# Kernel tuning notes

Measured on AMD Instinct MI355X. Metric: run time of the kernel, lower is better.

The kernel has to match this reference:

```python
import jax, jax.numpy as jnp
import numpy as np

N_NODES = 50000
N_EDGES = 500000
H = 128
C = 2


def setup_inputs() -> dict:
    key = jax.random.key(0)
    ks = jax.random.split(key, 8)
    node_repr = jax.random.normal(ks[0], (N_NODES, H), dtype=jnp.float32)
    src = jax.random.randint(ks[1], (N_EDGES,), 0, N_NODES, dtype=jnp.int32)
    dst = jax.random.randint(ks[2], (N_EDGES,), 0, N_NODES, dtype=jnp.int32)
    # Linear weights stored as (in, out); scaled like torch default init
    W1 = jax.random.normal(ks[3], (4 * H, 2 * H), dtype=jnp.float32) / np.sqrt(4 * H)
    b1 = jnp.zeros((2 * H,), dtype=jnp.float32)
    W2 = jax.random.normal(ks[4], (2 * H, H), dtype=jnp.float32) / np.sqrt(2 * H)
    b2 = jnp.zeros((H,), dtype=jnp.float32)
    W3 = jax.random.normal(ks[5], (H, C), dtype=jnp.float32) / np.sqrt(H)
    b3 = jnp.zeros((C,), dtype=jnp.float32)
    return {"node_repr": node_repr, "src": src, "dst": dst,
            "W1": W1, "b1": b1, "W2": W2, "b2": b2, "W3": W3, "b3": b3}


def reference(node_repr, src, dst, W1, b1, W2, b2, W3, b3):
    h_i = node_repr[src]                      # [E, H] gather
    h_j = node_repr[dst]                      # [E, H] gather
    diff = jnp.abs(h_i - h_j)
    product = h_i * h_j
    edge_input = jnp.concatenate([h_i, h_j, diff, product], axis=1)  # [E, 4H]
    x = jax.nn.relu(edge_input @ W1 + b1)     # [E, 2H]; dropout = identity (eval)
    x = jax.nn.relu(x @ W2 + b2)              # [E, H]
    return x @ W3 + b3                        # [E, C]
```

## Files before the change

### kernel.cpp

```cpp
#include <hip/hip_runtime.h>


#define H 128

typedef __bf16 bf16x8 __attribute__((ext_vector_type(8)));
typedef float f32x4 __attribute__((ext_vector_type(4)));

__device__ __forceinline__ unsigned short f2bf(float f) {
    unsigned u = __builtin_bit_cast(unsigned, f);
    u += 0x7FFFu + ((u >> 16) & 1u);
    return (unsigned short)(u >> 16);
}
__device__ __forceinline__ float bfhi(unsigned u) {
    return __builtin_bit_cast(float, u & 0xffff0000u);
}
__device__ __forceinline__ float bflo(unsigned u) {
    return __builtin_bit_cast(float, u << 16);
}
__device__ __forceinline__ unsigned pk2(float r0, float r1) {
    unsigned u0 = __builtin_bit_cast(unsigned, r0) + 0x8000u;
    unsigned u1 = __builtin_bit_cast(unsigned, r1) + 0x8000u;
    return __builtin_amdgcn_perm(u1, u0, 0x07060302u);
}
__device__ __forceinline__ unsigned comb(unsigned ua, unsigned ub, bool isdiff) {
    float a0 = bflo(ua), a1 = bfhi(ua);
    float b0 = bflo(ub), b1 = bfhi(ub);
    float r0 = isdiff ? fabsf(a0 - b0) : a0 * b0;
    float r1 = isdiff ? fabsf(a1 - b1) : a1 * b1;
    return pk2(r0, r1);
}
__device__ __forceinline__ unsigned short cvt1(float v) {
    unsigned u = __builtin_bit_cast(unsigned, v) + 0x8000u;
    return (unsigned short)(u >> 16);
}

__global__ void prep_node(const float* __restrict__ node, unsigned short* __restrict__ nbf) {
    int idx = blockIdx.x * 256 + threadIdx.x;
    const f32x4* p = (const f32x4*)(node) + idx;
    f32x4 v = *p;
    ushort4 w;
    w.x = f2bf(v.x); w.y = f2bf(v.y); w.z = f2bf(v.z); w.w = f2bf(v.w);
    *(ushort4*)(nbf + idx * 4) = w;
}

__global__ void prep_w1(const float* __restrict__ W1, unsigned short* __restrict__ W1P) {
    int o = blockIdx.x * 256 + threadIdx.x;
    int chunk = o >> 9;
    int g_nt = chunk >> 4;
    int ks = chunk & 15;
    int r = o & 511;
    int lane = r >> 3;
    int j = r & 7;
    int row = g_nt * 16 + (lane & 15);
    int k = ks * 32 + (lane >> 4) * 8 + j;
    W1P[o] = f2bf(W1[k * 256 + row]);
}

__global__ void prep_w2(const float* __restrict__ W2, unsigned short* __restrict__ W2P) {
    int o = blockIdx.x * 256 + threadIdx.x;
    int chunk = o >> 9;
    int g_nt = chunk >> 3;
    int ks = chunk & 7;
    int r = o & 511;
    int lane = r >> 3;
    int j = r & 7;
    int row = g_nt * 16 + (lane & 15);
    int k = ks * 32 + (lane >> 4) * 8 + j;
    W2P[o] = f2bf(W2[k * 128 + row]);
}

__launch_bounds__(256, 4)
__global__ void fused_mlp(const unsigned short* __restrict__ nbf,
                          const int* __restrict__ src,
                          const int* __restrict__ dst,
                          const unsigned short* __restrict__ W1P,
                          const float* __restrict__ b1,
                          const unsigned short* __restrict__ W2P,
                          const float* __restrict__ b2,
                          const float* __restrict__ W3,
                          const float* __restrict__ b3,
                          float* __restrict__ out,
                          int E) {
    __shared__ __align__(16) unsigned short sH[64 * 268];
    __shared__ __align__(16) float sW3[256];

    const int t = threadIdx.x;
    const int e0 = blockIdx.x * 64;

    const int lane = t & 63;
    const int wv = t >> 6;
    const int quad = lane >> 4;
    const int lrow = lane & 15;
    const int nb = wv * 64;
    const int nb2 = wv * 32;

    const unsigned short* w1b = W1P + wv * 32768 + lane * 8;
    const unsigned short* w2b = W2P + wv * 8192 + lane * 8;

    {
        int r = t >> 2;
        int q = t & 3;
        int e = e0 + r;
        int ec = e < E ? e : (E - 1);
        const unsigned short* hi = nbf + (long)src[ec] * H + q * 32;
        const unsigned short* hj = nbf + (long)dst[ec] * H + q * 32;
        unsigned short* rowp = sH + r * 268 + q * 32;
#pragma unroll
        for (int b = 0; b < 4; b++) {
            uint4 a = *(const uint4*)(hi + b * 8);
            uint4 c = *(const uint4*)(hj + b * 8);
            *(uint4*)(rowp + b * 8)       = a;
            *(uint4*)(rowp + 136 + b * 8) = c;
        }
        sW3[(t & 1) * 128 + (t >> 1)] = W3[t];
    }
    __syncthreads();

    f32x4 acc[4][4];
#pragma unroll
    for (int mt = 0; mt < 4; mt++)
#pragma unroll
        for (int nt = 0; nt < 4; nt++)
            acc[mt][nt] = (f32x4){0.f, 0.f, 0.f, 0.f};

    int aoff[4];
#pragma unroll
    for (int mt = 0; mt < 4; mt++) aoff[mt] = (mt * 16 + lrow) * 268 + quad * 8;

#pragma unroll 1
    for (int ks = 0; ks < 8; ks++) {
        const int ao = (ks < 4) ? ks * 32 : 136 + (ks - 4) * 32;
        bf16x8 bv[4], av[4];
#pragma unroll
        for (int nt = 0; nt < 4; nt++) bv[nt] = *(const bf16x8*)(w1b + nt * 8192 + ks * 512);
#pragma unroll
        for (int mt = 0; mt < 4; mt++) av[mt] = *(const bf16x8*)(sH + aoff[mt] + ao);
#pragma unroll
        for (int mt = 0; mt < 4; mt++)
#pragma unroll
            for (int nt = 0; nt < 4; nt++)
                acc[mt][nt] = __builtin_amdgcn_mfma_f32_16x16x32_bf16(av[mt], bv[nt], acc[mt][nt], 0, 0, 0);
    }

#pragma unroll 1
    for (int ks = 0; ks < 4; ks++) {
        bf16x8 bv[4];
#pragma unroll
        for (int nt = 0; nt < 4; nt++) bv[nt] = *(const bf16x8*)(w1b + nt * 8192 + (ks + 8) * 512);
#pragma unroll
        for (int mt = 0; mt < 4; mt++) {
            uint4 hu = *(const uint4*)(sH + aoff[mt] + ks * 32);
            uint4 ju = *(const uint4*)(sH + aoff[mt] + 136 + ks * 32);
            uint4 cv;
            cv.x = comb(hu.x, ju.x, true);  cv.y = comb(hu.y, ju.y, true);
            cv.z = comb(hu.z, ju.z, true);  cv.w = comb(hu.w, ju.w, true);
            bf16x8 av = __builtin_bit_cast(bf16x8, cv);
#pragma unroll
            for (int nt = 0; nt < 4; nt++)
                acc[mt][nt] = __builtin_amdgcn_mfma_f32_16x16x32_bf16(av, bv[nt], acc[mt][nt], 0, 0, 0);
        }
    }

#pragma unroll 1
    for (int ks = 0; ks < 4; ks++) {
        bf16x8 bv[4];
#pragma unroll
        for (int nt = 0; nt < 4; nt++) bv[nt] = *(const bf16x8*)(w1b + nt * 8192 + (ks + 12) * 512);
#pragma unroll
        for (int mt = 0; mt < 4; mt++) {
            uint4 hu = *(const uint4*)(sH + aoff[mt] + ks * 32);
            uint4 ju = *(const uint4*)(sH + aoff[mt] + 136 + ks * 32);
            uint4 cv;
            cv.x = comb(hu.x, ju.x, false); cv.y = comb(hu.y, ju.y, false);
            cv.z = comb(hu.z, ju.z, false); cv.w = comb(hu.w, ju.w, false);
            bf16x8 av = __builtin_bit_cast(bf16x8, cv);
#pragma unroll
            for (int nt = 0; nt < 4; nt++)
                acc[mt][nt] = __builtin_amdgcn_mfma_f32_16x16x32_bf16(av, bv[nt], acc[mt][nt], 0, 0, 0);
        }
    }

    float b1v[4];
#pragma unroll
    for (int nt = 0; nt < 4; nt++) b1v[nt] = b1[nb + nt * 16 + lrow];
    float b2v[2];
#pragma unroll
    for (int nt = 0; nt < 2; nt++) b2v[nt] = b2[nb2 + nt * 16 + lrow];

    __syncthreads();
    unsigned short* sx1 = sH;
#pragma unroll
    for (int mt = 0; mt < 4; mt++)
#pragma unroll
        for (int nt = 0; nt < 4; nt++)
#pragma unroll
            for (int i = 0; i < 4; i++) {
                int row = mt * 16 + quad * 4 + i;
                int col = nb + nt * 16 + lrow;
                float v = acc[mt][nt][i] + b1v[nt];
                v = v > 0.f ? v : 0.f;
                sx1[row * 268 + col] = cvt1(v);
            }
    __syncthreads();

    f32x4 acc2[4][2];
#pragma unroll
    for (int mt = 0; mt < 4; mt++)
#pragma unroll
        for (int nt = 0; nt < 2; nt++)
            acc2[mt][nt] = (f32x4){0.f, 0.f, 0.f, 0.f};

#pragma unroll 1
    for (int ks = 0; ks < 8; ks++) {
        bf16x8 bv2[2], av2[4];
#pragma unroll
        for (int nt = 0; nt < 2; nt++) bv2[nt] = *(const bf16x8*)(w2b + nt * 4096 + ks * 512);
#pragma unroll
        for (int mt = 0; mt < 4; mt++) av2[mt] = *(const bf16x8*)(sx1 + aoff[mt] + ks * 32);
#pragma unroll
        for (int mt = 0; mt < 4; mt++)
#pragma unroll
            for (int nt = 0; nt < 2; nt++)
                acc2[mt][nt] = __builtin_amdgcn_mfma_f32_16x16x32_bf16(av2[mt], bv2[nt], acc2[mt][nt], 0, 0, 0);
    }

    __syncthreads();
    unsigned short* sx2 = sH;
#pragma unroll
    for (int mt = 0; mt < 4; mt++)
#pragma unroll
        for (int nt = 0; nt < 2; nt++)
#pragma unroll
            for (int i = 0; i < 4; i++) {
                int row = mt * 16 + quad * 4 + i;
                int col = nb2 + nt * 16 + lrow;
                float v = acc2[mt][nt][i] + b2v[nt];
                v = v > 0.f ? v : 0.f;
                sx2[row * 140 + col] = cvt1(v);
            }
    __syncthreads();

    {
        int r = t >> 2;
        int c = t & 1;
        int h = (t >> 1) & 1;
        const unsigned short* xr = sx2 + r * 140 + h * 64;
        const float* w3c = sW3 + c * 128 + h * 64;
        float s = 0.f;
#pragma unroll
        for (int j = 0; j < 8; j++) {
            uint4 v = *(const uint4*)(xr + j * 8);
            f32x4 w0 = *(const f32x4*)(w3c + j * 8);
            f32x4 w1 = *(const f32x4*)(w3c + j * 8 + 4);
            s += bflo(v.x) * w0[0] + bfhi(v.x) * w0[1]
               + bflo(v.y) * w0[2] + bfhi(v.y) * w0[3]
               + bflo(v.z) * w1[0] + bfhi(v.z) * w1[1]
               + bflo(v.w) * w1[2] + bfhi(v.w) * w1[3];
        }
        s += __shfl_xor(s, 2);
        int e = e0 + r;
        if (h == 0 && e < E) out[e * 2 + c] = s + b3[c];
    }
}

extern "C" void kernel_launch(void* const* d_in, const int* in_sizes, int n_in,
                              void* d_out, int out_size, void* d_ws, size_t ws_size,
                              hipStream_t stream) {
    const float* node = (const float*)d_in[0];
    const int* src    = (const int*)d_in[1];
    const int* dst    = (const int*)d_in[2];
    const float* W1   = (const float*)d_in[3];
    const float* b1   = (const float*)d_in[4];
    const float* W2   = (const float*)d_in[5];
    const float* b2   = (const float*)d_in[6];
    const float* W3   = (const float*)d_in[7];
    const float* b3   = (const float*)d_in[8];
    float* out = (float*)d_out;
    const int NN = in_sizes[0] / H;
    const int E = in_sizes[1];

    unsigned short* W1P = (unsigned short*)d_ws;
    unsigned short* W2P = W1P + 512 * 256;
    unsigned short* NBF = W2P + 256 * 128;

    hipLaunchKernelGGL(prep_node, dim3((NN * H / 4 + 255) / 256), dim3(256), 0, stream, node, NBF);
    hipLaunchKernelGGL(prep_w1, dim3(512), dim3(256), 0, stream, W1, W1P);
    hipLaunchKernelGGL(prep_w2, dim3(128), dim3(256), 0, stream, W2, W2P);
    const int nblk = (E + 63) / 64;
    hipLaunchKernelGGL(fused_mlp, dim3(nblk), dim3(256), 0, stream,
                       NBF, src, dst, W1P, b1, W2P, b2, W3, b3, out, E);
}
```

Measured before the change: 359.2 us.

## Split MLP GEMMs across waves by edge rows instead of output columns

Each wave now owns 16 edge rows and computes every output column of both hidden layers, where before each wave owned a quarter of the columns for all 64 rows. Because a wave only reads and writes its own rows in shared memory, the barriers between layer 1, its activation writeback and layer 2 go away. The cost is weight reuse: each B fragment now feeds one MFMA instead of four, so every wave streams all of W1 and W2. Global and cache traffic for the weights per block grows about fourfold.

```diff
diff --git a/kernel.cpp b/kernel.cpp
--- a/kernel.cpp
+++ b/kernel.cpp
@@ -91,11 +91,9 @@
     const int wv = t >> 6;
     const int quad = lane >> 4;
     const int lrow = lane & 15;
-    const int nb = wv * 64;
-    const int nb2 = wv * 32;
-
-    const unsigned short* w1b = W1P + wv * 32768 + lane * 8;
-    const unsigned short* w2b = W2P + wv * 8192 + lane * 8;
+
+    const unsigned short* w1b = W1P + lane * 8;
+    const unsigned short* w2b = W2P + lane * 8;
 
     {
         int r = t >> 2;
@@ -116,135 +114,99 @@
     }
     __syncthreads();
 
-    f32x4 acc[4][4];
-#pragma unroll
-    for (int mt = 0; mt < 4; mt++)
-#pragma unroll
-        for (int nt = 0; nt < 4; nt++)
-            acc[mt][nt] = (f32x4){0.f, 0.f, 0.f, 0.f};
-
-    int aoff[4];
-#pragma unroll
-    for (int mt = 0; mt < 4; mt++) aoff[mt] = (mt * 16 + lrow) * 268 + quad * 8;
+    f32x4 acc[16];
+#pragma unroll
+    for (int nt = 0; nt < 16; nt++) acc[nt] = (f32x4){0.f, 0.f, 0.f, 0.f};
+
+    const int aoff = (wv * 16 + lrow) * 268 + quad * 8;
 
 #pragma unroll 1
     for (int ks = 0; ks < 8; ks++) {
         const int ao = (ks < 4) ? ks * 32 : 136 + (ks - 4) * 32;
-        bf16x8 bv[4], av[4];
-#pragma unroll
-        for (int nt = 0; nt < 4; nt++) bv[nt] = *(const bf16x8*)(w1b + nt * 8192 + ks * 512);
-#pragma unroll
-        for (int mt = 0; mt < 4; mt++) av[mt] = *(const bf16x8*)(sH + aoff[mt] + ao);
-#pragma unroll
-        for (int mt = 0; mt < 4; mt++)
-#pragma unroll
-            for (int nt = 0; nt < 4; nt++)
-                acc[mt][nt] = __builtin_amdgcn_mfma_f32_16x16x32_bf16(av[mt], bv[nt], acc[mt][nt], 0, 0, 0);
+        bf16x8 av = *(const bf16x8*)(sH + aoff + ao);
+#pragma unroll
+        for (int nt = 0; nt < 16; nt++) {
+            bf16x8 bv = *(const bf16x8*)(w1b + nt * 8192 + ks * 512);
+            acc[nt] = __builtin_amdgcn_mfma_f32_16x16x32_bf16(av, bv, acc[nt], 0, 0, 0);
+        }
     }
 
 #pragma unroll 1
     for (int ks = 0; ks < 4; ks++) {
-        bf16x8 bv[4];
-#pragma unroll
-        for (int nt = 0; nt < 4; nt++) bv[nt] = *(const bf16x8*)(w1b + nt * 8192 + (ks + 8) * 512);
-#pragma unroll
-        for (int mt = 0; mt < 4; mt++) {
-            uint4 hu = *(const uint4*)(sH + aoff[mt] + ks * 32);
-            uint4 ju = *(const uint4*)(sH + aoff[mt] + 136 + ks * 32);
-            uint4 cv;
-            cv.x = comb(hu.x, ju.x, true);  cv.y = comb(hu.y, ju.y, true);
-            cv.z = comb(hu.z, ju.z, true);  cv.w = comb(hu.w, ju.w, true);
-            bf16x8 av = __builtin_bit_cast(bf16x8, cv);
-#pragma unroll
-            for (int nt = 0; nt < 4; nt++)
-                acc[mt][nt] = __builtin_amdgcn_mfma_f32_16x16x32_bf16(av, bv[nt], acc[mt][nt], 0, 0, 0);
+        uint4 hu = *(const uint4*)(sH + aoff + ks * 32);
+        uint4 ju = *(const uint4*)(sH + aoff + 136 + ks * 32);
+        uint4 cv;
+        cv.x = comb(hu.x, ju.x, true);  cv.y = comb(hu.y, ju.y, true);
+        cv.z = comb(hu.z, ju.z, true);  cv.w = comb(hu.w, ju.w, true);
+        bf16x8 av = __builtin_bit_cast(bf16x8, cv);
+#pragma unroll
+        for (int nt = 0; nt < 16; nt++) {
+            bf16x8 bv = *(const bf16x8*)(w1b + nt * 8192 + (ks + 8) * 512);
+            acc[nt] = __builtin_amdgcn_mfma_f32_16x16x32_bf16(av, bv, acc[nt], 0, 0, 0);
         }
     }
 
 #pragma unroll 1
     for (int ks = 0; ks < 4; ks++) {
-        bf16x8 bv[4];
-#pragma unroll
-        for (int nt = 0; nt < 4; nt++) bv[nt] = *(const bf16x8*)(w1b + nt * 8192 + (ks + 12) * 512);
-#pragma unroll
-        for (int mt = 0; mt < 4; mt++) {
-            uint4 hu = *(const uint4*)(sH + aoff[mt] + ks * 32);
-            uint4 ju = *(const uint4*)(sH + aoff[mt] + 136 + ks * 32);
-            uint4 cv;
-            cv.x = comb(hu.x, ju.x, false); cv.y = comb(hu.y, ju.y, false);
-            cv.z = comb(hu.z, ju.z, false); cv.w = comb(hu.w, ju.w, false);
-            bf16x8 av = __builtin_bit_cast(bf16x8, cv);
-#pragma unroll
-            for (int nt = 0; nt < 4; nt++)
-                acc[mt][nt] = __builtin_amdgcn_mfma_f32_16x16x32_bf16(av, bv[nt], acc[mt][nt], 0, 0, 0);
-        }
-    }
-
-    float b1v[4];
-#pragma unroll
-    for (int nt = 0; nt < 4; nt++) b1v[nt] = b1[nb + nt * 16 + lrow];
-    float b2v[2];
-#pragma unroll
-    for (int nt = 0; nt < 2; nt++) b2v[nt] = b2[nb2 + nt * 16 + lrow];
-
-    __syncthreads();
+        uint4 hu = *(const uint4*)(sH + aoff + ks * 32);
+        uint4 ju = *(const uint4*)(sH + aoff + 136 + ks * 32);
+        uint4 cv;
+        cv.x = comb(hu.x, ju.x, false); cv.y = comb(hu.y, ju.y, false);
+        cv.z = comb(hu.z, ju.z, false); cv.w = comb(hu.w, ju.w, false);
+        bf16x8 av = __builtin_bit_cast(bf16x8, cv);
+#pragma unroll
+        for (int nt = 0; nt < 16; nt++) {
+            bf16x8 bv = *(const bf16x8*)(w1b + nt * 8192 + (ks + 12) * 512);
+            acc[nt] = __builtin_amdgcn_mfma_f32_16x16x32_bf16(av, bv, acc[nt], 0, 0, 0);
+        }
+    }
+
     unsigned short* sx1 = sH;
 #pragma unroll
-    for (int mt = 0; mt < 4; mt++)
-#pragma unroll
-        for (int nt = 0; nt < 4; nt++)
-#pragma unroll
-            for (int i = 0; i < 4; i++) {
-                int row = mt * 16 + quad * 4 + i;
-                int col = nb + nt * 16 + lrow;
-                float v = acc[mt][nt][i] + b1v[nt];
-                v = v > 0.f ? v : 0.f;
-                sx1[row * 268 + col] = cvt1(v);
-            }
-    __syncthreads();
-
-    f32x4 acc2[4][2];
-#pragma unroll
-    for (int mt = 0; mt < 4; mt++)
-#pragma unroll
-        for (int nt = 0; nt < 2; nt++)
-            acc2[mt][nt] = (f32x4){0.f, 0.f, 0.f, 0.f};
+    for (int nt = 0; nt < 16; nt++) {
+        float bb = b1[nt * 16 + lrow];
+#pragma unroll
+        for (int i = 0; i < 4; i++) {
+            int row = wv * 16 + quad * 4 + i;
+            float v = acc[nt][i] + bb;
+            v = v > 0.f ? v : 0.f;
+            sx1[row * 268 + nt * 16 + lrow] = cvt1(v);
+        }
+    }
+
+    f32x4 acc2[8];
+#pragma unroll
+    for (int nt = 0; nt < 8; nt++) acc2[nt] = (f32x4){0.f, 0.f, 0.f, 0.f};
 
 #pragma unroll 1
     for (int ks = 0; ks < 8; ks++) {
-        bf16x8 bv2[2], av2[4];
-#pragma unroll
-        for (int nt = 0; nt < 2; nt++) bv2[nt] = *(const bf16x8*)(w2b + nt * 4096 + ks * 512);
-#pragma unroll
-        for (int mt = 0; mt < 4; mt++) av2[mt] = *(const bf16x8*)(sx1 + aoff[mt] + ks * 32);
-#pragma unroll
-        for (int mt = 0; mt < 4; mt++)
-#pragma unroll
-            for (int nt = 0; nt < 2; nt++)
-                acc2[mt][nt] = __builtin_amdgcn_mfma_f32_16x16x32_bf16(av2[mt], bv2[nt], acc2[mt][nt], 0, 0, 0);
-    }
-
-    __syncthreads();
+        bf16x8 av2 = *(const bf16x8*)(sx1 + aoff + ks * 32);
+#pragma unroll
+        for (int nt = 0; nt < 8; nt++) {
+            bf16x8 bv2 = *(const bf16x8*)(w2b + nt * 4096 + ks * 512);
+            acc2[nt] = __builtin_amdgcn_mfma_f32_16x16x32_bf16(av2, bv2, acc2[nt], 0, 0, 0);
+        }
+    }
+
     unsigned short* sx2 = sH;
 #pragma unroll
-    for (int mt = 0; mt < 4; mt++)
-#pragma unroll
-        for (int nt = 0; nt < 2; nt++)
-#pragma unroll
-            for (int i = 0; i < 4; i++) {
-                int row = mt * 16 + quad * 4 + i;
-                int col = nb2 + nt * 16 + lrow;
-                float v = acc2[mt][nt][i] + b2v[nt];
-                v = v > 0.f ? v : 0.f;
-                sx2[row * 140 + col] = cvt1(v);
-            }
+    for (int nt = 0; nt < 8; nt++) {
+        float bb = b2[nt * 16 + lrow];
+#pragma unroll
+        for (int i = 0; i < 4; i++) {
+            int row = wv * 16 + quad * 4 + i;
+            float v = acc2[nt][i] + bb;
+            v = v > 0.f ? v : 0.f;
+            sx2[row * 268 + nt * 16 + lrow] = cvt1(v);
+        }
+    }
     __syncthreads();
 
     {
         int r = t >> 2;
         int c = t & 1;
         int h = (t >> 1) & 1;
-        const unsigned short* xr = sx2 + r * 140 + h * 64;
+        const unsigned short* xr = sH + r * 268 + h * 64;
         const float* w3c = sW3 + c * 128 + h * 64;
         float s = 0.f;
 #pragma unroll
```

After: 628.6 us. 1.75x slower.
